# Kernel tuning notes

Measured on AMD Instinct MI355X. Metric: run time of the kernel, lower is better.

Reference implementation:

```python
import jax, jax.numpy as jnp
import numpy as np

N_NODES = 50000
N_EDGES = 800000
D = 128          # node / edge / u feature dim
OUT = 128
N_GRAPHS = 64
IN1 = 4 * D      # 512
IN2 = D + OUT + D  # 384


def setup_inputs() -> dict:
    key = jax.random.key(0)
    ks = jax.random.split(key, 10)
    x = jax.random.normal(ks[0], (N_NODES, D), dtype=jnp.float32)
    edge_index = jax.random.randint(ks[1], (2, N_EDGES), 0, N_NODES, dtype=jnp.int64)
    edge_attr = jax.random.normal(ks[2], (N_EDGES, D), dtype=jnp.float32)
    u = jax.random.normal(ks[3], (N_GRAPHS, D), dtype=jnp.float32)
    batch = jnp.sort(jax.random.randint(ks[4], (N_NODES,), 0, N_GRAPHS, dtype=jnp.int64))
    # MLP params (Linear: y = x @ W.T + b), kaiming-ish scale
    W1 = jax.random.normal(ks[5], (OUT, IN1), dtype=jnp.float32) / np.sqrt(IN1)
    b1 = jnp.zeros((OUT,), dtype=jnp.float32)
    W2 = jax.random.normal(ks[6], (OUT, IN2), dtype=jnp.float32) / np.sqrt(IN2)
    b2 = jnp.zeros((OUT,), dtype=jnp.float32)
    return {"x": x, "edge_index": edge_index, "edge_attr": edge_attr,
            "u": u, "batch": batch, "W1": W1, "b1": b1, "W2": W2, "b2": b2}


def reference(x, edge_index, edge_attr, u, batch, W1, b1, W2, b2):
    src, dst = edge_index[0], edge_index[1]
    source_features = x[src]                  # [E, D]
    dest_features = x[dst]                    # [E, D]
    u_edge = u[batch[dst]]                    # [E, D]
    edge_input = jnp.concatenate([dest_features, source_features, edge_attr, u_edge], axis=1)  # [E, IN1]
    edge_messages = jax.nn.relu(edge_input @ W1.T + b1)  # [E, OUT]
    aggregated = jax.ops.segment_sum(edge_messages, dst, num_segments=x.shape[0])  # [N, OUT]
    u_expanded = u[batch]                     # [N, D]
    node_input = jnp.concatenate([x, aggregated, u_expanded], axis=1)  # [N, IN2]
    return jax.nn.relu(node_input @ W2.T + b2)  # [N, OUT]
```

## Files before the change

### kernel.cpp

```cpp
#include <hip/hip_runtime.h>
#include <stdint.h>

#define NNODES 50000
#define NEDGES 800000
#define DIM 128
#define IN1 512
#define IN2 384
#define NSB 196

typedef __attribute__((ext_vector_type(8))) short bf16x8;
typedef __attribute__((ext_vector_type(8))) unsigned short u16x8;
typedef __attribute__((ext_vector_type(4))) float f32x4;
typedef __attribute__((ext_vector_type(4))) uint32_t u32x4;

__device__ __forceinline__ unsigned short f2bf(float f) {
  union { float f; uint32_t u; } v; v.f = f;
  return (unsigned short)((v.u + 0x7FFFu + ((v.u >> 16) & 1u)) >> 16);
}
__device__ __forceinline__ float bf2f(unsigned short u) {
  union { uint32_t u; float f; } v; v.u = ((uint32_t)u) << 16;
  return v.f;
}
__device__ __forceinline__ uint32_t cvtpk(float lo, float hi) {
  uint32_t r;
  asm volatile("v_cvt_pk_bf16_f32 %0, %1, %2" : "=v"(r) : "v"(lo), "v"(hi));
  return r;
}

__device__ __forceinline__ void cvt8(const float* __restrict__ p, unsigned short* dst, int sidx) {
  float4 f0 = *(const float4*)(p);
  float4 f1 = *(const float4*)(p + 4);
  u16x8 o;
  o[0] = f2bf(f0.x); o[1] = f2bf(f0.y); o[2] = f2bf(f0.z); o[3] = f2bf(f0.w);
  o[4] = f2bf(f1.x); o[5] = f2bf(f1.y); o[6] = f2bf(f1.z); o[7] = f2bf(f1.w);
  *(u16x8*)(dst + sidx) = o;
}

__device__ __forceinline__ void mfma128(const unsigned short* As, const unsigned short* Bs,
                                        f32x4 acc[4][4], int wm, int wn, int l) {
#pragma unroll
  for (int kk = 0; kk < 4; ++kk) {
    bf16x8 a[4], b[4];
#pragma unroll
    for (int mi = 0; mi < 4; ++mi) {
      int row = wm * 64 + mi * 16 + (l & 15);
      int idx = (row * 128 + kk * 32 + (l >> 4) * 8) ^ ((row & 7) << 3);
      a[mi] = *(const bf16x8*)(As + idx);
    }
#pragma unroll
    for (int ni = 0; ni < 4; ++ni) {
      int nrow = wn * 64 + ni * 16 + (l & 15);
      int idx = (nrow * 128 + kk * 32 + (l >> 4) * 8) ^ ((nrow & 7) << 3);
      b[ni] = *(const bf16x8*)(Bs + idx);
    }
#pragma unroll
    for (int mi = 0; mi < 4; ++mi)
#pragma unroll
      for (int ni = 0; ni < 4; ++ni)
        acc[mi][ni] = __builtin_amdgcn_mfma_f32_16x16x32_bf16(a[mi], b[ni], acc[mi][ni], 0, 0, 0);
  }
}

__global__ void zero_kernel(float4* __restrict__ a, int n4, int* __restrict__ c, int nc) {
  int i = blockIdx.x * 256 + threadIdx.x;
  int stride = gridDim.x * 256;
  for (int k = i; k < n4; k += stride) a[k] = float4{0.f, 0.f, 0.f, 0.f};
  for (int k = i; k < nc; k += stride) c[k] = 0;
}

__global__ void wconv_p0_kernel(const float* __restrict__ W1, const float* __restrict__ W2,
                                const float* __restrict__ u, const float* __restrict__ b1,
                                const float* __restrict__ b2,
                                unsigned short* __restrict__ Wt,
                                float* __restrict__ Ud, float* __restrict__ Uc) {
  int b = blockIdx.x;
  if (b < 320) {
    int t = b * 256 + threadIdx.x;
    int tile = t >> 14, rem = t & 16383, n = rem >> 7, k = rem & 127;
    float v = (tile < 3) ? W1[(size_t)n * IN1 + tile * 128 + k]
                         : W2[(size_t)n * IN2 + (tile - 3) * 128 + k];
    int lin = ((n * 128 + (k & ~7)) ^ ((n & 7) << 3)) | (k & 7);
    Wt[tile * 16384 + lin] = f2bf(v);
  } else {
    int g = (b - 320) * 2 + (threadIdx.x >> 7);
    int c = threadIdx.x & 127;
    const float* ur = u + (size_t)g * DIM;
    const float* w1 = W1 + (size_t)c * IN1 + 384;
    const float* w2 = W2 + (size_t)c * IN2 + 256;
    float s1 = b1[c], s2 = b2[c];
    for (int k = 0; k < DIM; ++k) { float uv = ur[k]; s1 += uv * w1[k]; s2 += uv * w2[k]; }
    Ud[g * DIM + c] = s1;
    Uc[g * DIM + c] = s2;
  }
}

__global__ __launch_bounds__(256, 2) void p1_kernel(
    const float* __restrict__ x, const int* __restrict__ batch,
    const unsigned short* __restrict__ Wt,
    const float* __restrict__ Ud, const float* __restrict__ Uc,
    unsigned short* __restrict__ Xad, unsigned short* __restrict__ Xb,
    unsigned short* __restrict__ Yx) {
  __shared__ __align__(16) unsigned short As[128 * 128];
  __shared__ __align__(16) unsigned short Bs[128 * 128];
  const int t = threadIdx.x, l = t & 63, w = t >> 6, wm = w >> 1, wn = w & 1;
  const int n0 = blockIdx.x * 128, r = t >> 1, h = t & 1;
  const int swz = (r & 7) << 3;
  {
    int n = n0 + r; if (n >= NNODES) n = NNODES - 1;
    const float* rowp = x + (size_t)n * DIM + h * 64;
#pragma unroll
    for (int i = 0; i < 8; ++i) cvt8(rowp + i * 8, As, (r * 128 + h * 64 + i * 8) ^ swz);
  }
#pragma unroll
  for (int p = 0; p < 3; ++p) {
    __syncthreads();
    {
      const u16x8* wsrc = (const u16x8*)(Wt + (size_t)((p == 2) ? 3 : p) * 16384);
      u16x8* bdst = (u16x8*)Bs;
#pragma unroll
      for (int i = 0; i < 8; ++i) bdst[t + i * 256] = wsrc[t + i * 256];
    }
    __syncthreads();
    f32x4 acc[4][4] = {};
    mfma128(As, Bs, acc, wm, wn, l);
#pragma unroll
    for (int mi = 0; mi < 4; ++mi)
#pragma unroll
      for (int rr = 0; rr < 4; ++rr) {
        int m = wm * 64 + mi * 16 + (l >> 4) * 4 + rr;
        int n = n0 + m;
        if (n < NNODES) {
          int g = batch[n];
#pragma unroll
          for (int ni = 0; ni < 4; ++ni) {
            int col = wn * 64 + ni * 16 + (l & 15);
            float v = acc[mi][ni][rr];
            if (p == 0)      Xad[(size_t)n * DIM + col] = f2bf(v + Ud[g * DIM + col]);
            else if (p == 1) Xb [(size_t)n * DIM + col] = f2bf(v);
            else             Yx [(size_t)n * DIM + col] = f2bf(v + Uc[g * DIM + col]);
          }
        }
      }
  }
}

__global__ void hist_kernel(const int* __restrict__ dstI, int* __restrict__ count) {
  int e = blockIdx.x * 256 + threadIdx.x;
  if (e < NEDGES) atomicAdd(&count[dstI[e]], 1);
}

__global__ void scan1_kernel(const int* __restrict__ count, int* __restrict__ bsum) {
  __shared__ int ws[4];
  int i = blockIdx.x * 256 + threadIdx.x;
  int v = (i < NNODES) ? count[i] : 0;
  int l = threadIdx.x & 63;
#pragma unroll
  for (int off = 32; off > 0; off >>= 1) v += __shfl_down(v, off);
  if (l == 0) ws[threadIdx.x >> 6] = v;
  __syncthreads();
  if (threadIdx.x == 0) bsum[blockIdx.x] = ws[0] + ws[1] + ws[2] + ws[3];
}

__global__ void scan2_kernel(const int* __restrict__ bsum, int* __restrict__ bpre) {
  __shared__ int s[256];
  int i = threadIdx.x;
  int v = (i < NSB) ? bsum[i] : 0;
  s[i] = v; __syncthreads();
  for (int off = 1; off < 256; off <<= 1) {
    int u = (i >= off) ? s[i - off] : 0;
    __syncthreads();
    s[i] += u;
    __syncthreads();
  }
  if (i < NSB) bpre[i] = s[i] - v;
}

__global__ void scan3_kernel(const int* __restrict__ count, const int* __restrict__ bpre,
                             int* __restrict__ rowptr) {
  __shared__ int s[256];
  int b = blockIdx.x, i = threadIdx.x, g = b * 256 + i;
  int v = (g < NNODES) ? count[g] : 0;
  s[i] = v; __syncthreads();
  for (int off = 1; off < 256; off <<= 1) {
    int u = (i >= off) ? s[i - off] : 0;
    __syncthreads();
    s[i] += u;
    __syncthreads();
  }
  if (g < NNODES) rowptr[g] = bpre[b] + s[i] - v;
}

__global__ void scatter_kernel(const int* __restrict__ srcI, const int* __restrict__ dstI,
                               int* __restrict__ rowptr, uint64_t* __restrict__ esd) {
  int e = blockIdx.x * 256 + threadIdx.x;
  if (e < NEDGES) {
    int d = dstI[e], s = srcI[e];
    int pos = atomicAdd(&rowptr[d], 1);
    esd[pos] = ((uint64_t)(uint32_t)e << 32) | ((uint32_t)s << 16) | (uint32_t)d;
  }
}

__global__ __launch_bounds__(512, 6) void edge2_kernel(
    const float* __restrict__ ea, const uint64_t* __restrict__ esd,
    const unsigned short* __restrict__ W1cs,
    const unsigned short* __restrict__ Xad, const unsigned short* __restrict__ Xb,
    float* __restrict__ agg) {
  __shared__ __align__(16) unsigned short smem[24576];
  __shared__ int dlds[64];
  __shared__ int segs[66];
  __shared__ int nsegS;
  unsigned short* As  = smem;
  unsigned short* Bs  = smem + 8192;
  unsigned short* Xbs = smem;
  float* Ms = (float*)(smem + 8192);

  const int t = threadIdx.x, l = t & 63, w = t >> 6;
  const int wm = w >> 2, wn = w & 3;
  int bid = blockIdx.x;
  const int nwg = NEDGES / 64, q = nwg >> 3, r8 = nwg & 7;
  int xcd = bid & 7, off = bid >> 3;
  int wg = (xcd < r8) ? xcd * (q + 1) + off : r8 * (q + 1) + (xcd - r8) * q + off;
  const int p0 = wg * 64;
  const int r = t >> 3, o = t & 7;

  {
    const u16x8* wsrc = (const u16x8*)W1cs;
    u16x8* bdst = (u16x8*)Bs;
#pragma unroll
    for (int i = 0; i < 4; ++i) bdst[t + i * 512] = wsrc[t + i * 512];
  }
  if (t < 64) {
    uint64_t vv = esd[p0 + t];
    int d = (int)(vv & 0xFFFF);
    dlds[t] = d;
    int dp = __shfl_up(d, 1);
    bool st = (t == 0) || (d != dp);
    uint64_t m = __ballot(st);
    int rank = (t == 0) ? 0 : __popcll(m & ((1ull << t) - 1ull));
    if (st) segs[rank] = t;
    if (t == 0) { int ns = __popcll(m); nsegS = ns; segs[ns] = 64; }
  }
  uint64_t v = esd[p0 + r];
  {
    int e = (int)(v >> 32);
    const float* rowp = ea + (size_t)e * DIM + o * 16;
    float4 f0 = *(const float4*)(rowp);
    float4 f1 = *(const float4*)(rowp + 4);
    float4 f2 = *(const float4*)(rowp + 8);
    float4 f3 = *(const float4*)(rowp + 12);
    const int swz = (r & 7) << 3;
    u32x4 g0 = {cvtpk(f0.x, f0.y), cvtpk(f0.z, f0.w), cvtpk(f1.x, f1.y), cvtpk(f1.z, f1.w)};
    u32x4 g1 = {cvtpk(f2.x, f2.y), cvtpk(f2.z, f2.w), cvtpk(f3.x, f3.y), cvtpk(f3.z, f3.w)};
    *(u32x4*)(As + ((r * 128 + o * 16) ^ swz)) = g0;
    *(u32x4*)(As + ((r * 128 + o * 16 + 8) ^ swz)) = g1;
  }
  u16x8 xv0, xv1;
  {
    int s = (int)((v >> 16) & 0xFFFF);
    const u16x8* xr = (const u16x8*)(Xb + (size_t)s * DIM);
    xv0 = xr[o * 2];
    xv1 = xr[o * 2 + 1];
  }
  __syncthreads();

  f32x4 acc[2][2] = {};
#pragma unroll
  for (int kk = 0; kk < 4; ++kk) {
    bf16x8 a[2], b[2];
#pragma unroll
    for (int mi = 0; mi < 2; ++mi) {
      int row = wm * 32 + mi * 16 + (l & 15);
      int idx = (row * 128 + kk * 32 + (l >> 4) * 8) ^ ((row & 7) << 3);
      a[mi] = *(const bf16x8*)(As + idx);
    }
#pragma unroll
    for (int ni = 0; ni < 2; ++ni) {
      int n = wn * 32 + ni * 16 + (l & 15);
      int idx = (n * 128 + kk * 32 + (l >> 4) * 8) ^ ((n & 7) << 3);
      b[ni] = *(const bf16x8*)(Bs + idx);
    }
#pragma unroll
    for (int mi = 0; mi < 2; ++mi)
#pragma unroll
      for (int ni = 0; ni < 2; ++ni)
        acc[mi][ni] = __builtin_amdgcn_mfma_f32_16x16x32_bf16(a[mi], b[ni], acc[mi][ni], 0, 0, 0);
  }
  __syncthreads();

  {
    int sw = ((r >> 2) & 3) << 1;
    u16x8* xb8 = (u16x8*)Xbs;
    xb8[r * 16 + ((o * 2) ^ sw)] = xv0;
    xb8[r * 16 + ((o * 2 + 1) ^ sw)] = xv1;
  }
  __syncthreads();

#pragma unroll
  for (int mi = 0; mi < 2; ++mi)
#pragma unroll
    for (int rr = 0; rr < 4; ++rr) {
      int m = wm * 32 + mi * 16 + (l >> 4) * 4 + rr;
      int d = dlds[m];
      const unsigned short* xa = Xad + (size_t)d * DIM;
      int cs = ((m >> 2) & 3) << 3;
      int cx = ((m >> 2) & 3) << 4;
#pragma unroll
      for (int ni = 0; ni < 2; ++ni) {
        int col = wn * 32 + ni * 16 + (l & 15);
        float vv = acc[mi][ni][rr] + bf2f(xa[col]) + bf2f(Xbs[m * 128 + (col ^ cx)]);
        Ms[m * 128 + (col ^ cs)] = fmaxf(vv, 0.0f);
      }
    }
  __syncthreads();

  {
    int nseg = nsegS;
    for (int sc = w; sc < nseg; sc += 8) {
      int beg = segs[sc], end = segs[sc + 1];
      int d = dlds[beg];
      float* arow = agg + (size_t)d * DIM;
      bool interior = (sc > 0) && (sc < nseg - 1);
#pragma unroll
      for (int cc = 0; cc < 2; ++cc) {
        int col = l + cc * 64;
        float s = 0.0f;
        for (int r2 = beg; r2 < end; ++r2)
          s += Ms[r2 * 128 + (col ^ (((r2 >> 2) & 3) << 3))];
        if (interior) arow[col] = s;
        else unsafeAtomicAdd(arow + col, s);
      }
    }
  }
}

__global__ __launch_bounds__(256, 2) void edge_kernel(
    const float* __restrict__ ea, const int* __restrict__ srcI, const int* __restrict__ dstI,
    const unsigned short* __restrict__ W1cs,
    const unsigned short* __restrict__ Xad, const unsigned short* __restrict__ Xb,
    float* __restrict__ agg) {
  __shared__ __align__(16) unsigned short As[128 * 128];
  __shared__ __align__(16) unsigned short Bs[128 * 128];
  const int t = threadIdx.x, l = t & 63, w = t >> 6, wm = w >> 1, wn = w & 1;
  const int e0 = blockIdx.x * 128, r = t >> 1, h = t & 1;
  const int swz = (r & 7) << 3;
  {
    const float* rowp = ea + (size_t)(e0 + r) * DIM + h * 64;
#pragma unroll
    for (int i = 0; i < 8; ++i) cvt8(rowp + i * 8, As, (r * 128 + h * 64 + i * 8) ^ swz);
  }
  {
    const u16x8* wsrc = (const u16x8*)W1cs;
    u16x8* bdst = (u16x8*)Bs;
#pragma unroll
    for (int i = 0; i < 8; ++i) bdst[t + i * 256] = wsrc[t + i * 256];
  }
  __syncthreads();
  f32x4 acc[4][4] = {};
  mfma128(As, Bs, acc, wm, wn, l);
#pragma unroll
  for (int mi = 0; mi < 4; ++mi)
#pragma unroll
    for (int rr = 0; rr < 4; ++rr) {
      int m = wm * 64 + mi * 16 + (l >> 4) * 4 + rr;
      int e = e0 + m;
      int d = dstI[e], s = srcI[e];
      const unsigned short* xa = Xad + (size_t)d * DIM;
      const unsigned short* xb = Xb + (size_t)s * DIM;
      float* ag = agg + (size_t)d * DIM;
#pragma unroll
      for (int ni = 0; ni < 4; ++ni) {
        int col = wn * 64 + ni * 16 + (l & 15);
        float v = acc[mi][ni][rr] + bf2f(xa[col]) + bf2f(xb[col]);
        unsafeAtomicAdd(ag + col, fmaxf(v, 0.0f));
      }
    }
}

__global__ __launch_bounds__(256, 2) void node_kernel(
    const float* __restrict__ agg, const unsigned short* __restrict__ Wt,
    const unsigned short* __restrict__ Yx, float* __restrict__ out) {
  __shared__ __align__(16) unsigned short As[128 * 128];
  __shared__ __align__(16) unsigned short Bs[128 * 128];
  const int t = threadIdx.x, l = t & 63, w = t >> 6, wm = w >> 1, wn = w & 1;
  const int n0 = blockIdx.x * 128, r = t >> 1, h = t & 1;
  const int swz = (r & 7) << 3;
  {
    int n = n0 + r; if (n >= NNODES) n = NNODES - 1;
    const float* rowp = agg + (size_t)n * DIM + h * 64;
#pragma unroll
    for (int i = 0; i < 8; ++i) cvt8(rowp + i * 8, As, (r * 128 + h * 64 + i * 8) ^ swz);
  }
  {
    const u16x8* wsrc = (const u16x8*)(Wt + (size_t)4 * 16384);
    u16x8* bdst = (u16x8*)Bs;
#pragma unroll
    for (int i = 0; i < 8; ++i) bdst[t + i * 256] = wsrc[t + i * 256];
  }
  __syncthreads();
  f32x4 acc[4][4] = {};
  mfma128(As, Bs, acc, wm, wn, l);
#pragma unroll
  for (int mi = 0; mi < 4; ++mi)
#pragma unroll
    for (int rr = 0; rr < 4; ++rr) {
      int m = wm * 64 + mi * 16 + (l >> 4) * 4 + rr;
      int n = n0 + m;
      if (n < NNODES) {
        float* orow = out + (size_t)n * DIM;
#pragma unroll
        for (int ni = 0; ni < 4; ++ni) {
          int col = wn * 64 + ni * 16 + (l & 15);
          float v = acc[mi][ni][rr] + bf2f(Yx[(size_t)n * DIM + col]);
          orow[col] = fmaxf(v, 0.0f);
        }
      }
    }
}

extern "C" void kernel_launch(void* const* d_in, const int* in_sizes, int n_in,
                              void* d_out, int out_size, void* d_ws, size_t ws_size,
                              hipStream_t stream) {
  const float* x   = (const float*)d_in[0];
  const int* ei    = (const int*)d_in[1];
  const float* ea  = (const float*)d_in[2];
  const float* u   = (const float*)d_in[3];
  const int* batch = (const int*)d_in[4];
  const float* W1  = (const float*)d_in[5];
  const float* b1  = (const float*)d_in[6];
  const float* W2  = (const float*)d_in[7];
  const float* b2  = (const float*)d_in[8];
  float* out = (float*)d_out;
  const int* srcI = ei;
  const int* dstI = ei + NEDGES;

  const size_t XAD_B = (size_t)NNODES * DIM * 2;
  const size_t U_B   = (size_t)64 * DIM * 4;
  const size_t WT_B  = (size_t)5 * 16384 * 2;
  const size_t ESD_B = (size_t)NEDGES * 8;
  const size_t CNT_B = (size_t)(NNODES + 64) * 4;
  const size_t BS_B  = 4096;
  const size_t need_base = 3 * XAD_B + 2 * U_B + WT_B;
  const size_t need_sort = need_base + ESD_B + 2 * CNT_B + 2 * BS_B;

  char* p = (char*)d_ws;
  unsigned short* Xad = (unsigned short*)p; p += XAD_B;
  unsigned short* Xb  = (unsigned short*)p; p += XAD_B;
  unsigned short* Yx  = (unsigned short*)p; p += XAD_B;
  float* Ud = (float*)p; p += U_B;
  float* Uc = (float*)p; p += U_B;
  unsigned short* Wt = (unsigned short*)p; p += WT_B;
  uint64_t* esd = (uint64_t*)p; p += ESD_B;
  int* count  = (int*)p; p += CNT_B;
  int* rowptr = (int*)p; p += CNT_B;
  int* bsum = (int*)p; p += BS_B;
  int* bpre = (int*)p;

  float* agg = out;
  const int nAgg4 = NNODES * DIM / 4;

  if (ws_size >= need_sort) {
    zero_kernel<<<2048, 256, 0, stream>>>((float4*)agg, nAgg4, count, NNODES + 64);
    hist_kernel<<<(NEDGES + 255) / 256, 256, 0, stream>>>(dstI, count);
    scan1_kernel<<<NSB, 256, 0, stream>>>(count, bsum);
    scan2_kernel<<<1, 256, 0, stream>>>(bsum, bpre);
    scan3_kernel<<<NSB, 256, 0, stream>>>(count, bpre, rowptr);
    scatter_kernel<<<(NEDGES + 255) / 256, 256, 0, stream>>>(srcI, dstI, rowptr, esd);
    wconv_p0_kernel<<<352, 256, 0, stream>>>(W1, W2, u, b1, b2, Wt, Ud, Uc);
    p1_kernel<<<(NNODES + 127) / 128, 256, 0, stream>>>(x, batch, Wt, Ud, Uc, Xad, Xb, Yx);
    edge2_kernel<<<NEDGES / 64, 512, 0, stream>>>(ea, esd, Wt + 2 * 16384, Xad, Xb, agg);
    node_kernel<<<(NNODES + 127) / 128, 256, 0, stream>>>(agg, Wt, Yx, out);
  } else if (ws_size >= need_base) {
    zero_kernel<<<2048, 256, 0, stream>>>((float4*)agg, nAgg4, (int*)Ud, 0);
    wconv_p0_kernel<<<352, 256, 0, stream>>>(W1, W2, u, b1, b2, Wt, Ud, Uc);
    p1_kernel<<<(NNODES + 127) / 128, 256, 0, stream>>>(x, batch, Wt, Ud, Uc, Xad, Xb, Yx);
    edge_kernel<<<NEDGES / 128, 256, 0, stream>>>(ea, srcI, dstI, Wt + 2 * 16384, Xad, Xb, agg);
    node_kernel<<<(NNODES + 127) / 128, 256, 0, stream>>>(agg, Wt, Yx, out);
  }
}
```

Before: 323.3 us.

## Make edge kernel persistent over five tiles with register-prefetched gathers

Each workgroup of the edge kernel now processes five consecutive 64-edge tiles instead of one. It loads the W1 slice into LDS once per workgroup and prefetches the next tile's edge_attr rows, source features and sorted-edge metadata into registers while the current tile computes. The intermediate message buffer is now stored as bf16, not fp32, so As, Bs and Xbs get separate LDS regions, and launch bounds drop from 6 to 4 waves. The aim is to amortise the weight load and hide gather latency, at the cost of lower occupancy, more registers, and bf16 rounding of messages before the segment sum.

```diff
diff --git a/kernel.cpp b/kernel.cpp
--- a/kernel.cpp
+++ b/kernel.cpp
@@ -7,6 +7,7 @@
 #define IN1 512
 #define IN2 384
 #define NSB 196
+#define PT 5
 
 typedef __attribute__((ext_vector_type(8))) short bf16x8;
 typedef __attribute__((ext_vector_type(8))) unsigned short u16x8;
@@ -200,27 +201,26 @@
   }
 }
 
-__global__ __launch_bounds__(512, 6) void edge2_kernel(
+__global__ __launch_bounds__(512, 4) void edge2_kernel(
     const float* __restrict__ ea, const uint64_t* __restrict__ esd,
     const unsigned short* __restrict__ W1cs,
     const unsigned short* __restrict__ Xad, const unsigned short* __restrict__ Xb,
     float* __restrict__ agg) {
-  __shared__ __align__(16) unsigned short smem[24576];
+  __shared__ __align__(16) unsigned short Bs[16384];
+  __shared__ __align__(16) unsigned short As[8192];
+  __shared__ __align__(16) unsigned short Xbs[8192];
   __shared__ int dlds[64];
   __shared__ int segs[66];
   __shared__ int nsegS;
-  unsigned short* As  = smem;
-  unsigned short* Bs  = smem + 8192;
-  unsigned short* Xbs = smem;
-  float* Ms = (float*)(smem + 8192);
+  unsigned short* Ms = As;
 
   const int t = threadIdx.x, l = t & 63, w = t >> 6;
   const int wm = w >> 2, wn = w & 3;
   int bid = blockIdx.x;
-  const int nwg = NEDGES / 64, q = nwg >> 3, r8 = nwg & 7;
+  const int nwg = NEDGES / (64 * PT), q = nwg >> 3, r8 = nwg & 7;
   int xcd = bid & 7, off = bid >> 3;
   int wg = (xcd < r8) ? xcd * (q + 1) + off : r8 * (q + 1) + (xcd - r8) * q + off;
-  const int p0 = wg * 64;
+  const int base = wg * (64 * PT);
   const int r = t >> 3, o = t & 7;
 
   {
@@ -229,107 +229,125 @@
 #pragma unroll
     for (int i = 0; i < 4; ++i) bdst[t + i * 512] = wsrc[t + i * 512];
   }
-  if (t < 64) {
-    uint64_t vv = esd[p0 + t];
-    int d = (int)(vv & 0xFFFF);
-    dlds[t] = d;
-    int dp = __shfl_up(d, 1);
-    bool st = (t == 0) || (d != dp);
-    uint64_t m = __ballot(st);
-    int rank = (t == 0) ? 0 : __popcll(m & ((1ull << t) - 1ull));
-    if (st) segs[rank] = t;
-    if (t == 0) { int ns = __popcll(m); nsegS = ns; segs[ns] = 64; }
-  }
-  uint64_t v = esd[p0 + r];
-  {
-    int e = (int)(v >> 32);
+
+  uint64_t v0 = esd[base + r];
+  uint64_t vn = (PT > 1) ? esd[base + 64 + r] : 0;
+  uint64_t vn2;
+  float4 a0, a1, a2, a3;
+  u16x8 x0, x1;
+  {
+    int e = (int)(v0 >> 32);
     const float* rowp = ea + (size_t)e * DIM + o * 16;
-    float4 f0 = *(const float4*)(rowp);
-    float4 f1 = *(const float4*)(rowp + 4);
-    float4 f2 = *(const float4*)(rowp + 8);
-    float4 f3 = *(const float4*)(rowp + 12);
-    const int swz = (r & 7) << 3;
-    u32x4 g0 = {cvtpk(f0.x, f0.y), cvtpk(f0.z, f0.w), cvtpk(f1.x, f1.y), cvtpk(f1.z, f1.w)};
-    u32x4 g1 = {cvtpk(f2.x, f2.y), cvtpk(f2.z, f2.w), cvtpk(f3.x, f3.y), cvtpk(f3.z, f3.w)};
-    *(u32x4*)(As + ((r * 128 + o * 16) ^ swz)) = g0;
-    *(u32x4*)(As + ((r * 128 + o * 16 + 8) ^ swz)) = g1;
-  }
-  u16x8 xv0, xv1;
-  {
-    int s = (int)((v >> 16) & 0xFFFF);
+    a0 = *(const float4*)(rowp);
+    a1 = *(const float4*)(rowp + 4);
+    a2 = *(const float4*)(rowp + 8);
+    a3 = *(const float4*)(rowp + 12);
+    int s = (int)((v0 >> 16) & 0xFFFF);
     const u16x8* xr = (const u16x8*)(Xb + (size_t)s * DIM);
-    xv0 = xr[o * 2];
-    xv1 = xr[o * 2 + 1];
-  }
-  __syncthreads();
-
-  f32x4 acc[2][2] = {};
-#pragma unroll
-  for (int kk = 0; kk < 4; ++kk) {
-    bf16x8 a[2], b[2];
-#pragma unroll
-    for (int mi = 0; mi < 2; ++mi) {
-      int row = wm * 32 + mi * 16 + (l & 15);
-      int idx = (row * 128 + kk * 32 + (l >> 4) * 8) ^ ((row & 7) << 3);
-      a[mi] = *(const bf16x8*)(As + idx);
-    }
-#pragma unroll
-    for (int ni = 0; ni < 2; ++ni) {
-      int n = wn * 32 + ni * 16 + (l & 15);
-      int idx = (n * 128 + kk * 32 + (l >> 4) * 8) ^ ((n & 7) << 3);
-      b[ni] = *(const bf16x8*)(Bs + idx);
-    }
+    x0 = xr[o * 2];
+    x1 = xr[o * 2 + 1];
+  }
+
+  for (int tt = 0; tt < PT; ++tt) {
+    const int p0 = base + tt * 64;
+    if (o == 0) dlds[r] = (int)(v0 & 0xFFFF);
+    {
+      const int swz = (r & 7) << 3;
+      u32x4 g0 = {cvtpk(a0.x, a0.y), cvtpk(a0.z, a0.w), cvtpk(a1.x, a1.y), cvtpk(a1.z, a1.w)};
+      u32x4 g1 = {cvtpk(a2.x, a2.y), cvtpk(a2.z, a2.w), cvtpk(a3.x, a3.y), cvtpk(a3.z, a3.w)};
+      *(u32x4*)(As + ((r * 128 + o * 16) ^ swz)) = g0;
+      *(u32x4*)(As + ((r * 128 + o * 16 + 8) ^ swz)) = g1;
+      int sw = ((r >> 2) & 3) << 1;
+      u16x8* xb8 = (u16x8*)Xbs;
+      xb8[r * 16 + ((o * 2) ^ sw)] = x0;
+      xb8[r * 16 + ((o * 2 + 1) ^ sw)] = x1;
+    }
+    if (tt < PT - 1) {
+      int e = (int)(vn >> 32);
+      const float* rowp = ea + (size_t)e * DIM + o * 16;
+      a0 = *(const float4*)(rowp);
+      a1 = *(const float4*)(rowp + 4);
+      a2 = *(const float4*)(rowp + 8);
+      a3 = *(const float4*)(rowp + 12);
+      int s = (int)((vn >> 16) & 0xFFFF);
+      const u16x8* xr = (const u16x8*)(Xb + (size_t)s * DIM);
+      x0 = xr[o * 2];
+      x1 = xr[o * 2 + 1];
+    }
+    if (tt < PT - 2) vn2 = esd[base + (tt + 2) * 64 + r];
+    __syncthreads();
+
+    if (w == 0) {
+      int d = dlds[l];
+      int dp = __shfl_up(d, 1);
+      bool st = (l == 0) || (d != dp);
+      uint64_t m = __ballot(st);
+      int rank = (l == 0) ? 0 : __popcll(m & ((1ull << l) - 1ull));
+      if (st) segs[rank] = l;
+      if (l == 0) { int ns = __popcll(m); nsegS = ns; segs[ns] = 64; }
+    }
+
+    f32x4 acc[2][2] = {};
+#pragma unroll
+    for (int kk = 0; kk < 4; ++kk) {
+      bf16x8 a[2], b[2];
+#pragma unroll
+      for (int mi = 0; mi < 2; ++mi) {
+        int row = wm * 32 + mi * 16 + (l & 15);
+        int idx = (row * 128 + kk * 32 + (l >> 4) * 8) ^ ((row & 7) << 3);
+        a[mi] = *(const bf16x8*)(As + idx);
+      }
+#pragma unroll
+      for (int ni = 0; ni < 2; ++ni) {
+        int n = wn * 32 + ni * 16 + (l & 15);
+        int idx = (n * 128 + kk * 32 + (l >> 4) * 8) ^ ((n & 7) << 3);
+        b[ni] = *(const bf16x8*)(Bs + idx);
+      }
+#pragma unroll
+      for (int mi = 0; mi < 2; ++mi)
+#pragma unroll
+        for (int ni = 0; ni < 2; ++ni)
+          acc[mi][ni] = __builtin_amdgcn_mfma_f32_16x16x32_bf16(a[mi], b[ni], acc[mi][ni], 0, 0, 0);
+    }
+    __syncthreads();
+
 #pragma unroll
     for (int mi = 0; mi < 2; ++mi)
 #pragma unroll
-      for (int ni = 0; ni < 2; ++ni)
-        acc[mi][ni] = __builtin_amdgcn_mfma_f32_16x16x32_bf16(a[mi], b[ni], acc[mi][ni], 0, 0, 0);
-  }
-  __syncthreads();
-
-  {
-    int sw = ((r >> 2) & 3) << 1;
-    u16x8* xb8 = (u16x8*)Xbs;
-    xb8[r * 16 + ((o * 2) ^ sw)] = xv0;
-    xb8[r * 16 + ((o * 2 + 1) ^ sw)] = xv1;
-  }
-  __syncthreads();
-
-#pragma unroll
-  for (int mi = 0; mi < 2; ++mi)
-#pragma unroll
-    for (int rr = 0; rr < 4; ++rr) {
-      int m = wm * 32 + mi * 16 + (l >> 4) * 4 + rr;
-      int d = dlds[m];
-      const unsigned short* xa = Xad + (size_t)d * DIM;
-      int cs = ((m >> 2) & 3) << 3;
-      int cx = ((m >> 2) & 3) << 4;
-#pragma unroll
-      for (int ni = 0; ni < 2; ++ni) {
-        int col = wn * 32 + ni * 16 + (l & 15);
-        float vv = acc[mi][ni][rr] + bf2f(xa[col]) + bf2f(Xbs[m * 128 + (col ^ cx)]);
-        Ms[m * 128 + (col ^ cs)] = fmaxf(vv, 0.0f);
-      }
-    }
-  __syncthreads();
-
-  {
-    int nseg = nsegS;
-    for (int sc = w; sc < nseg; sc += 8) {
-      int beg = segs[sc], end = segs[sc + 1];
-      int d = dlds[beg];
-      float* arow = agg + (size_t)d * DIM;
-      bool interior = (sc > 0) && (sc < nseg - 1);
-#pragma unroll
-      for (int cc = 0; cc < 2; ++cc) {
-        int col = l + cc * 64;
-        float s = 0.0f;
-        for (int r2 = beg; r2 < end; ++r2)
-          s += Ms[r2 * 128 + (col ^ (((r2 >> 2) & 3) << 3))];
-        if (interior) arow[col] = s;
-        else unsafeAtomicAdd(arow + col, s);
-      }
-    }
+      for (int rr = 0; rr < 4; ++rr) {
+        int m = wm * 32 + mi * 16 + (l >> 4) * 4 + rr;
+        int d = dlds[m];
+        const unsigned short* xa = Xad + (size_t)d * DIM;
+        int cx = ((m >> 2) & 3) << 4;
+#pragma unroll
+        for (int ni = 0; ni < 2; ++ni) {
+          int col = wn * 32 + ni * 16 + (l & 15);
+          float vv = acc[mi][ni][rr] + bf2f(xa[col]) + bf2f(Xbs[m * 128 + (col ^ cx)]);
+          Ms[m * 128 + (col ^ cx)] = f2bf(fmaxf(vv, 0.0f));
+        }
+      }
+    __syncthreads();
+
+    {
+      int nseg = nsegS;
+      for (int sc = w; sc < nseg; sc += 8) {
+        int beg = segs[sc], end = segs[sc + 1];
+        int d = dlds[beg];
+        float* arow = agg + (size_t)d * DIM;
+        bool interior = (sc > 0) && (sc < nseg - 1);
+#pragma unroll
+        for (int cc = 0; cc < 2; ++cc) {
+          int col = l + cc * 64;
+          float s = 0.0f;
+          for (int r2 = beg; r2 < end; ++r2)
+            s += bf2f(Ms[r2 * 128 + (col ^ (((r2 >> 2) & 3) << 4))]);
+          if (interior) arow[col] = s;
+          else unsafeAtomicAdd(arow + col, s);
+        }
+      }
+    }
+    __syncthreads();
+    v0 = vn; vn = vn2;
   }
 }
 
@@ -467,7 +485,7 @@
     scatter_kernel<<<(NEDGES + 255) / 256, 256, 0, stream>>>(srcI, dstI, rowptr, esd);
     wconv_p0_kernel<<<352, 256, 0, stream>>>(W1, W2, u, b1, b2, Wt, Ud, Uc);
     p1_kernel<<<(NNODES + 127) / 128, 256, 0, stream>>>(x, batch, Wt, Ud, Uc, Xad, Xb, Yx);
-    edge2_kernel<<<NEDGES / 64, 512, 0, stream>>>(ea, esd, Wt + 2 * 16384, Xad, Xb, agg);
+    edge2_kernel<<<NEDGES / (64 * PT), 512, 0, stream>>>(ea, esd, Wt + 2 * 16384, Xad, Xb, agg);
     node_kernel<<<(NNODES + 127) / 128, 256, 0, stream>>>(agg, Wt, Yx, out);
   } else if (ws_size >= need_base) {
     zero_kernel<<<2048, 256, 0, stream>>>((float4*)agg, nAgg4, (int*)Ud, 0);
```

After: 367.1 us. 13.6% more time.
